# Kernel tuning notes

Measured on AMD Instinct MI355X. Metric: run time of the kernel, lower is better.

The kernel has to match this reference:

```python
import jax, jax.numpy as jnp
import numpy as np

D_IN = 768
D_OUT = 768
NUM_HEADS = 12
HEAD_DIM = D_OUT // NUM_HEADS


def setup_inputs() -> dict:
    key = jax.random.key(0)
    ks = jax.random.split(key, 6)
    s = 1.0 / np.sqrt(D_IN)
    X = jax.random.normal(ks[0], (4, 2048, D_IN), dtype=jnp.float32)
    Wq = jax.random.uniform(ks[1], (D_IN, D_OUT), jnp.float32, -s, s)
    Wk = jax.random.uniform(ks[2], (D_IN, D_OUT), jnp.float32, -s, s)
    Wv = jax.random.uniform(ks[3], (D_IN, D_OUT), jnp.float32, -s, s)
    Wo = jax.random.uniform(ks[4], (D_OUT, D_OUT), jnp.float32, -s, s)
    bo = jax.random.uniform(ks[5], (D_OUT,), jnp.float32, -s, s)
    return {"X": X, "Wq": Wq, "Wk": Wk, "Wv": Wv, "Wo": Wo, "bo": bo}


def reference(X, Wq, Wk, Wv, Wo, bo):
    b, n, _ = X.shape
    # QKV projections, split heads -> [b, h, n, d]
    def split(t):
        return t.reshape(b, n, NUM_HEADS, HEAD_DIM).transpose(0, 2, 1, 3)
    q = split(X @ Wq)
    k = split(X @ Wk)
    v = split(X @ Wv)
    scores = jnp.einsum('bhqd,bhkd->bhqk', q, k) / np.sqrt(HEAD_DIM).astype(np.float32)
    causal = jnp.triu(jnp.ones((n, n), dtype=bool), k=1)
    scores = jnp.where(causal, -jnp.inf, scores)
    attn = jax.nn.softmax(scores, axis=-1)  # dropout p=0 -> identity
    ctx = jnp.einsum('bhqk,bhkd->bhqd', attn, v)
    ctx = ctx.transpose(0, 2, 1, 3).reshape(b, n, D_OUT)
    return ctx @ Wo + bo
```

## Files before the change

kernel.cpp:

```cpp
#include <hip/hip_runtime.h>
#include <stdint.h>

#define B_  4
#define N_  2048
#define D_  768
#define H_  12
#define HD_ 64
#define M_  (B_*N_)

typedef short bf8 __attribute__((ext_vector_type(8)));
typedef float f32x4 __attribute__((ext_vector_type(4)));

static __device__ __forceinline__ unsigned short f2bf(float f) {
    unsigned u = __float_as_uint(f);
    unsigned r = u + 0x7fffu + ((u >> 16) & 1u);
    return (unsigned short)(r >> 16);
}

static __device__ __forceinline__ unsigned pk2bf(float f0, float f1) {
    return ((__float_as_uint(f1) + 0x8000u) & 0xFFFF0000u) |
           ((__float_as_uint(f0) + 0x8000u) >> 16);
}

#if __has_builtin(__builtin_amdgcn_exp2f)
#define EXP2(x) __builtin_amdgcn_exp2f(x)
#else
#define EXP2(x) exp2f(x)
#endif

#define GLOAD_LDS16(gptr, lptr)                                                   \
    __builtin_amdgcn_global_load_lds(                                             \
        (const __attribute__((address_space(1))) void*)(gptr),                    \
        (__attribute__((address_space(3))) void*)(lptr), 16, 0, 0)

#define QSCALE 0.1803368801111204f

__global__ __launch_bounds__(256) void convert_x(const float* __restrict__ X,
                                                 unsigned short* __restrict__ Xb) {
    const size_t i = ((size_t)blockIdx.x * 256 + threadIdx.x) * 8;
    const float4 a = *(const float4*)(X + i);
    const float4 b = *(const float4*)(X + i + 4);
    ushort4 lo, hi;
    lo.x = f2bf(a.x); lo.y = f2bf(a.y); lo.z = f2bf(a.z); lo.w = f2bf(a.w);
    hi.x = f2bf(b.x); hi.y = f2bf(b.y); hi.z = f2bf(b.z); hi.w = f2bf(b.w);
    *(ushort4*)(Xb + i)     = lo;
    *(ushort4*)(Xb + i + 4) = hi;
}

__global__ __launch_bounds__(256) void transpose_w(
    const float* __restrict__ Wq, const float* __restrict__ Wk,
    const float* __restrict__ Wv, const float* __restrict__ Wo,
    unsigned short* __restrict__ Wqt, unsigned short* __restrict__ Wkt,
    unsigned short* __restrict__ Wvt, unsigned short* __restrict__ Wot)
{
    __shared__ float tile[32][33];
    const int z = blockIdx.z;
    const float* W = (z == 0) ? Wq : (z == 1) ? Wk : (z == 2) ? Wv : Wo;
    unsigned short* Wt = (z == 0) ? Wqt : (z == 1) ? Wkt : (z == 2) ? Wvt : Wot;
    const int k0 = blockIdx.x * 32, n0 = blockIdx.y * 32;
    const int tx = threadIdx.x & 31, ty = threadIdx.x >> 5;
    #pragma unroll
    for (int i = 0; i < 4; ++i)
        tile[ty + 8 * i][tx] = W[(size_t)(k0 + ty + 8 * i) * D_ + n0 + tx];
    __syncthreads();
    #pragma unroll
    for (int i = 0; i < 4; ++i)
        Wt[(size_t)(n0 + ty + 8 * i) * D_ + k0 + tx] = f2bf(tile[tx][ty + 8 * i]);
}

__global__ __launch_bounds__(256) void qkv_mfma(
    const unsigned short* __restrict__ Xb,
    const unsigned short* __restrict__ Wqt, const unsigned short* __restrict__ Wkt,
    const unsigned short* __restrict__ Wvt,
    unsigned short* __restrict__ Qb, unsigned short* __restrict__ Kb,
    unsigned short* __restrict__ Vt)
{
    __shared__ unsigned short As[128 * 32];
    __shared__ unsigned short Bs[128 * 32];

    const int t = threadIdx.x;
    const int wave = t >> 6, lane = t & 63;
    const int col = lane & 15, quad = lane >> 4;
    const int wm = (wave & 1) * 64, wn = (wave >> 1) * 64;

    const int m0 = blockIdx.x * 128;
    const int n0 = blockIdx.y * 128;
    const int mat = blockIdx.z;
    const unsigned short* Wt = (mat == 0) ? Wqt : (mat == 1) ? Wkt : Wvt;

    const unsigned short* Ag0 = Xb + (size_t)(m0 + (t >> 2)) * D_ + (t & 3) * 8;
    const unsigned short* Ag1 = Ag0 + (size_t)64 * D_;
    const unsigned short* Bg0 = Wt + (size_t)(n0 + (t >> 2)) * D_ + (t & 3) * 8;
    const unsigned short* Bg1 = Bg0 + (size_t)64 * D_;
    unsigned short* AsW0 = As + wave * 512;
    unsigned short* AsW1 = As + 2048 + wave * 512;
    unsigned short* BsW0 = Bs + wave * 512;
    unsigned short* BsW1 = Bs + 2048 + wave * 512;

    f32x4 acc[4][4] = {};

    for (int k0 = 0; k0 < D_; k0 += 32) {
        __syncthreads();
        GLOAD_LDS16(Ag0 + k0, AsW0);
        GLOAD_LDS16(Ag1 + k0, AsW1);
        GLOAD_LDS16(Bg0 + k0, BsW0);
        GLOAD_LDS16(Bg1 + k0, BsW1);
        __syncthreads();

        bf8 a[4], b[4];
        #pragma unroll
        for (int i = 0; i < 4; ++i)
            a[i] = *(const bf8*)(As + (wm + i * 16 + col) * 32 + quad * 8);
        #pragma unroll
        for (int j = 0; j < 4; ++j)
            b[j] = *(const bf8*)(Bs + (wn + j * 16 + col) * 32 + quad * 8);
        #pragma unroll
        for (int i = 0; i < 4; ++i)
            #pragma unroll
            for (int j = 0; j < 4; ++j)
                acc[i][j] = __builtin_amdgcn_mfma_f32_16x16x32_bf16(a[i], b[j], acc[i][j], 0, 0, 0);
    }

    if (mat != 2) {
        unsigned short* Out = (mat == 0) ? Qb : Kb;
        const float qsc = (mat == 0) ? QSCALE : 1.0f;
        #pragma unroll
        for (int j = 0; j < 4; ++j) {
            const int n = n0 + wn + j * 16 + col;
            const int h = n >> 6, d = n & 63;
            #pragma unroll
            for (int i = 0; i < 4; ++i) {
                const int mb = m0 + wm + i * 16 + quad * 4;
                const int bb = mb >> 11, nn = mb & (N_ - 1);
                unsigned short* op = Out + ((size_t)(bb * H_ + h) * N_ + nn) * HD_ + d;
                #pragma unroll
                for (int r = 0; r < 4; ++r) op[(size_t)r * HD_] = f2bf(acc[i][j][r] * qsc);
            }
        }
    } else {
        #pragma unroll
        for (int j = 0; j < 4; ++j) {
            const int n = n0 + wn + j * 16 + col;
            const int h = n >> 6, d = n & 63;
            #pragma unroll
            for (int i = 0; i < 4; ++i) {
                const int mb = m0 + wm + i * 16 + quad * 4;
                const int bb = mb >> 11, nn = mb & (N_ - 1);
                ushort4 pk;
                pk.x = f2bf(acc[i][j][0]); pk.y = f2bf(acc[i][j][1]);
                pk.z = f2bf(acc[i][j][2]); pk.w = f2bf(acc[i][j][3]);
                *(ushort4*)(Vt + ((size_t)(bb * H_ + h) * HD_ + d) * N_ + nn) = pk;
            }
        }
    }
}

#define PS 72

static __device__ __forceinline__ void qk_softmax(
    const bf8 (&ka)[4][2], bf8 qb0, bf8 qb1,
    int k0, int q, bool mask, float& lpart,
    unsigned short* Pw, int col, int quad)
{
    f32x4 s[4] = {};
    #pragma unroll
    for (int kc = 0; kc < 4; ++kc) {
        s[kc] = __builtin_amdgcn_mfma_f32_16x16x32_bf16(ka[kc][0], qb0, s[kc], 0, 0, 0);
        s[kc] = __builtin_amdgcn_mfma_f32_16x16x32_bf16(ka[kc][1], qb1, s[kc], 0, 0, 0);
    }

    float p[4][4];
    if (mask) {
        #pragma unroll
        for (int kc = 0; kc < 4; ++kc)
            #pragma unroll
            for (int r = 0; r < 4; ++r) {
                const int key = k0 + kc * 16 + quad * 4 + r;
                p[kc][r] = EXP2((key > q) ? -INFINITY : s[kc][r]);
            }
    } else {
        #pragma unroll
        for (int kc = 0; kc < 4; ++kc)
            #pragma unroll
            for (int r = 0; r < 4; ++r) p[kc][r] = EXP2(s[kc][r]);
    }

    #pragma unroll
    for (int kc = 0; kc < 4; ++kc)
        #pragma unroll
        for (int r = 0; r < 4; ++r) lpart += p[kc][r];

    #pragma unroll
    for (int kc = 0; kc < 4; ++kc) {
        uint2 pk;
        pk.x = pk2bf(p[kc][0], p[kc][1]);
        pk.y = pk2bf(p[kc][2], p[kc][3]);
        *(uint2*)(Pw + col * PS + kc * 16 + quad * 4) = pk;
    }
}

static __device__ __forceinline__ void pv_acc(
    const unsigned short* Pw, const bf8 (&va)[4][2],
    f32x4 (&o)[4], int col, int quad)
{
    const bf8 pb0 = *(const bf8*)(Pw + col * PS + quad * 8);
    const bf8 pb1 = *(const bf8*)(Pw + col * PS + 32 + quad * 8);
    #pragma unroll
    for (int dc = 0; dc < 4; ++dc) {
        o[dc] = __builtin_amdgcn_mfma_f32_16x16x32_bf16(va[dc][0], pb0, o[dc], 0, 0, 0);
        o[dc] = __builtin_amdgcn_mfma_f32_16x16x32_bf16(va[dc][1], pb1, o[dc], 0, 0, 0);
    }
}

__global__ __launch_bounds__(256, 3) void attn_mfma(
    const unsigned short* __restrict__ Qb,
    const unsigned short* __restrict__ Kb,
    const unsigned short* __restrict__ Vt,
    unsigned short* __restrict__ Ctxb)
{
    __shared__ unsigned short Kl[64 * PS];
    __shared__ unsigned short Vl[64 * PS];
    __shared__ unsigned short Pl[4][16 * PS];

    const int t = threadIdx.x;
    const int wave = t >> 6;
    const int lane = t & 63;
    const int col  = lane & 15;
    const int quad = lane >> 4;

    const int bid = blockIdx.x;
    const int bh  = bid >> 4;
    const int x   = bid & 15;
    const int tl  = x, th = 31 - x;
    const int q0L = tl * 64 + wave * 16;
    const int q0H = th * 64 + wave * 16;
    const int qL  = q0L + col;
    const int qH  = q0H + col;

    const unsigned short* Kp = Kb + (size_t)bh * N_ * HD_;
    const unsigned short* Vp = Vt + (size_t)bh * HD_ * N_;
    const unsigned short* QpL = Qb + ((size_t)bh * N_ + q0L) * HD_;
    const unsigned short* QpH = Qb + ((size_t)bh * N_ + q0H) * HD_;

    const bf8 qbL0 = *(const bf8*)(QpL + (size_t)col * HD_ + quad * 8);
    const bf8 qbL1 = *(const bf8*)(QpL + (size_t)col * HD_ + 32 + quad * 8);
    const bf8 qbH0 = *(const bf8*)(QpH + (size_t)col * HD_ + quad * 8);
    const bf8 qbH1 = *(const bf8*)(QpH + (size_t)col * HD_ + 32 + quad * 8);

    f32x4 oL[4] = {}, oH[4] = {};
    float lL = 0.f, lH = 0.f;

    unsigned short* Pw = &Pl[wave][0];

    const int srow = t >> 3;
    const int scol = (t & 7) * 8;
    const unsigned short* Kg = Kp + (size_t)srow * HD_ + scol;
    const unsigned short* Vg = Vp + (size_t)srow * N_ + scol;
    unsigned short* KlD0 = Kl + srow * PS + scol;
    unsigned short* KlD1 = Kl + (srow + 32) * PS + scol;
    unsigned short* VlD0 = Vl + srow * PS + scol;
    unsigned short* VlD1 = Vl + (srow + 32) * PS + scol;

    uint4 kr0 = *(const uint4*)(Kg);
    uint4 kr1 = *(const uint4*)(Kg + (size_t)32 * HD_);
    uint4 vr0 = *(const uint4*)(Vg);
    uint4 vr1 = *(const uint4*)(Vg + (size_t)32 * N_);

    const int iters = 32 - x;
    for (int kt = 0; kt < iters; ++kt) {
        const int k0 = kt * 64;
        const bool actL = (kt <= tl);

        *(uint4*)KlD0 = kr0;
        *(uint4*)KlD1 = kr1;
        *(uint4*)VlD0 = vr0;
        *(uint4*)VlD1 = vr1;
        __syncthreads();

        if (kt + 1 < iters) {
            const size_t k1 = (size_t)(k0 + 64);
            kr0 = *(const uint4*)(Kg + k1 * HD_);
            kr1 = *(const uint4*)(Kg + (k1 + 32) * HD_);
            vr0 = *(const uint4*)(Vg + k1);
            vr1 = *(const uint4*)(Vg + (size_t)32 * N_ + k1);
        }

        bf8 ka[4][2];
        #pragma unroll
        for (int kc = 0; kc < 4; ++kc) {
            ka[kc][0] = *(const bf8*)(Kl + (kc * 16 + col) * PS + quad * 8);
            ka[kc][1] = *(const bf8*)(Kl + (kc * 16 + col) * PS + 32 + quad * 8);
        }

        qk_softmax(ka, qbH0, qbH1, k0, qH, kt == th, lH, Pw, col, quad);

        bf8 va[4][2];
        #pragma unroll
        for (int dc = 0; dc < 4; ++dc) {
            va[dc][0] = *(const bf8*)(Vl + (dc * 16 + col) * PS + quad * 8);
            va[dc][1] = *(const bf8*)(Vl + (dc * 16 + col) * PS + 32 + quad * 8);
        }

        pv_acc(Pw, va, oH, col, quad);

        if (actL) {
            qk_softmax(ka, qbL0, qbL1, k0, qL, kt == tl, lL, Pw, col, quad);
            pv_acc(Pw, va, oL, col, quad);
        }

        __syncthreads();
    }

    const int b = bh / H_;
    const int h = bh % H_;
    {
        float l = lH;
        l += __shfl_xor(l, 16, 64);
        l += __shfl_xor(l, 32, 64);
        const float inv = 1.0f / l;
        unsigned short* cp = Ctxb + ((size_t)(b * N_ + qH)) * D_ + h * HD_;
        #pragma unroll
        for (int dc = 0; dc < 4; ++dc) {
            uint2 pk;
            pk.x = pk2bf(oH[dc][0] * inv, oH[dc][1] * inv);
            pk.y = pk2bf(oH[dc][2] * inv, oH[dc][3] * inv);
            *(uint2*)(cp + dc * 16 + quad * 4) = pk;
        }
    }
    {
        float l = lL;
        l += __shfl_xor(l, 16, 64);
        l += __shfl_xor(l, 32, 64);
        const float inv = 1.0f / l;
        unsigned short* cp = Ctxb + ((size_t)(b * N_ + qL)) * D_ + h * HD_;
        #pragma unroll
        for (int dc = 0; dc < 4; ++dc) {
            uint2 pk;
            pk.x = pk2bf(oL[dc][0] * inv, oL[dc][1] * inv);
            pk.y = pk2bf(oL[dc][2] * inv, oL[dc][3] * inv);
            *(uint2*)(cp + dc * 16 + quad * 4) = pk;
        }
    }
}

__global__ __launch_bounds__(256) void out_mfma(
    const unsigned short* __restrict__ Ctxb,
    const unsigned short* __restrict__ Wot,
    const float* __restrict__ bo,
    float* __restrict__ Out)
{
    __shared__ unsigned short As[128 * 32];
    __shared__ unsigned short Bs[128 * 32];

    const int t = threadIdx.x;
    const int wave = t >> 6, lane = t & 63;
    const int col = lane & 15, quad = lane >> 4;
    const int wm = (wave & 1) * 64, wn = (wave >> 1) * 64;

    const int m0 = blockIdx.x * 128;
    const int n0 = blockIdx.y * 128;

    const unsigned short* Ag0 = Ctxb + (size_t)(m0 + (t >> 2)) * D_ + (t & 3) * 8;
    const unsigned short* Ag1 = Ag0 + (size_t)64 * D_;
    const unsigned short* Bg0 = Wot + (size_t)(n0 + (t >> 2)) * D_ + (t & 3) * 8;
    const unsigned short* Bg1 = Bg0 + (size_t)64 * D_;
    unsigned short* AsW0 = As + wave * 512;
    unsigned short* AsW1 = As + 2048 + wave * 512;
    unsigned short* BsW0 = Bs + wave * 512;
    unsigned short* BsW1 = Bs + 2048 + wave * 512;

    f32x4 acc[4][4] = {};

    for (int k0 = 0; k0 < D_; k0 += 32) {
        __syncthreads();
        GLOAD_LDS16(Ag0 + k0, AsW0);
        GLOAD_LDS16(Ag1 + k0, AsW1);
        GLOAD_LDS16(Bg0 + k0, BsW0);
        GLOAD_LDS16(Bg1 + k0, BsW1);
        __syncthreads();

        bf8 a[4], b[4];
        #pragma unroll
        for (int i = 0; i < 4; ++i)
            a[i] = *(const bf8*)(As + (wm + i * 16 + col) * 32 + quad * 8);
        #pragma unroll
        for (int j = 0; j < 4; ++j)
            b[j] = *(const bf8*)(Bs + (wn + j * 16 + col) * 32 + quad * 8);
        #pragma unroll
        for (int i = 0; i < 4; ++i)
            #pragma unroll
            for (int j = 0; j < 4; ++j)
                acc[i][j] = __builtin_amdgcn_mfma_f32_16x16x32_bf16(a[i], b[j], acc[i][j], 0, 0, 0);
    }

    #pragma unroll
    for (int j = 0; j < 4; ++j) {
        const int n = n0 + wn + j * 16 + col;
        const float bias = bo[n];
        #pragma unroll
        for (int i = 0; i < 4; ++i) {
            const int mb = m0 + wm + i * 16 + quad * 4;
            #pragma unroll
            for (int r = 0; r < 4; ++r)
                Out[(size_t)(mb + r) * D_ + n] = acc[i][j][r] + bias;
        }
    }
}

extern "C" void kernel_launch(void* const* d_in, const int* in_sizes, int n_in,
                              void* d_out, int out_size, void* d_ws, size_t ws_size,
                              hipStream_t stream) {
    const float* X  = (const float*)d_in[0];
    const float* Wq = (const float*)d_in[1];
    const float* Wk = (const float*)d_in[2];
    const float* Wv = (const float*)d_in[3];
    const float* Wo = (const float*)d_in[4];
    const float* bo = (const float*)d_in[5];
    float* out = (float*)d_out;

    const size_t elems = (size_t)M_ * D_;
    const size_t welems = (size_t)D_ * D_;
    unsigned short* Xb  = (unsigned short*)d_ws;
    unsigned short* Wqt = Xb + elems;
    unsigned short* Wkt = Wqt + welems;
    unsigned short* Wvt = Wkt + welems;
    unsigned short* Wot = Wvt + welems;
    unsigned short* Qb  = Wot + welems;
    unsigned short* Kb  = Qb + elems;
    unsigned short* Vt  = Kb + elems;
    unsigned short* Ctxb = Xb;

    convert_x<<<dim3(elems / 2048), 256, 0, stream>>>(X, Xb);
    transpose_w<<<dim3(24, 24, 4), 256, 0, stream>>>(Wq, Wk, Wv, Wo, Wqt, Wkt, Wvt, Wot);

    qkv_mfma<<<dim3(M_ / 128, D_ / 128, 3), 256, 0, stream>>>(Xb, Wqt, Wkt, Wvt, Qb, Kb, Vt);

    attn_mfma<<<dim3(B_ * H_ * 16), 256, 0, stream>>>(Qb, Kb, Vt, Ctxb);

    out_mfma<<<dim3(M_ / 128, D_ / 128), 256, 0, stream>>>(Ctxb, Wot, bo, out);
}
```

Measured before the change: 216.7 us.

## Double-buffer attention K/V tiles, widen GEMM K-step, and vectorize epilogue stores

The attention kernel now double-buffers K and V in LDS with a two-stage register prefetch, which removes the trailing barrier per key tile. The QKV and output GEMMs load 64-wide K slices per barrier pair, and for Q/K and the output GEMM they swap the MFMA operands so each lane holds consecutive output columns, allowing 8-byte bf16 and 16-byte float4 stores instead of scalar strided stores. MFMA sections are also wrapped in s_setprio to favor matrix issue. This doubles LDS use in both attention and GEMM kernels, which may reduce occupancy.

```diff
diff --git a/kernel.cpp b/kernel.cpp
--- a/kernel.cpp
+++ b/kernel.cpp
@@ -75,8 +75,8 @@
     unsigned short* __restrict__ Qb, unsigned short* __restrict__ Kb,
     unsigned short* __restrict__ Vt)
 {
-    __shared__ unsigned short As[128 * 32];
-    __shared__ unsigned short Bs[128 * 32];
+    __shared__ unsigned short As[8192];
+    __shared__ unsigned short Bs[8192];
 
     const int t = threadIdx.x;
     const int wave = t >> 6, lane = t & 63;
@@ -87,54 +87,69 @@
     const int n0 = blockIdx.y * 128;
     const int mat = blockIdx.z;
     const unsigned short* Wt = (mat == 0) ? Wqt : (mat == 1) ? Wkt : Wvt;
-
-    const unsigned short* Ag0 = Xb + (size_t)(m0 + (t >> 2)) * D_ + (t & 3) * 8;
-    const unsigned short* Ag1 = Ag0 + (size_t)64 * D_;
-    const unsigned short* Bg0 = Wt + (size_t)(n0 + (t >> 2)) * D_ + (t & 3) * 8;
-    const unsigned short* Bg1 = Bg0 + (size_t)64 * D_;
-    unsigned short* AsW0 = As + wave * 512;
-    unsigned short* AsW1 = As + 2048 + wave * 512;
-    unsigned short* BsW0 = Bs + wave * 512;
-    unsigned short* BsW1 = Bs + 2048 + wave * 512;
+    const bool sw = (mat != 2);
+
+    const unsigned short* Ag = Xb + (size_t)(m0 + (t >> 2)) * D_ + (t & 3) * 8;
+    const unsigned short* Bg = Wt + (size_t)(n0 + (t >> 2)) * D_ + (t & 3) * 8;
+    unsigned short* AsD = As + t * 8;
+    unsigned short* BsD = Bs + t * 8;
 
     f32x4 acc[4][4] = {};
 
-    for (int k0 = 0; k0 < D_; k0 += 32) {
+    for (int k0 = 0; k0 < D_; k0 += 64) {
         __syncthreads();
-        GLOAD_LDS16(Ag0 + k0, AsW0);
-        GLOAD_LDS16(Ag1 + k0, AsW1);
-        GLOAD_LDS16(Bg0 + k0, BsW0);
-        GLOAD_LDS16(Bg1 + k0, BsW1);
+        GLOAD_LDS16(Ag + k0,                        AsD);
+        GLOAD_LDS16(Ag + k0 + 32,                   AsD + 4096);
+        GLOAD_LDS16(Ag + (size_t)64 * D_ + k0,      AsD + 2048);
+        GLOAD_LDS16(Ag + (size_t)64 * D_ + k0 + 32, AsD + 6144);
+        GLOAD_LDS16(Bg + k0,                        BsD);
+        GLOAD_LDS16(Bg + k0 + 32,                   BsD + 4096);
+        GLOAD_LDS16(Bg + (size_t)64 * D_ + k0,      BsD + 2048);
+        GLOAD_LDS16(Bg + (size_t)64 * D_ + k0 + 32, BsD + 6144);
         __syncthreads();
 
-        bf8 a[4], b[4];
-        #pragma unroll
-        for (int i = 0; i < 4; ++i)
-            a[i] = *(const bf8*)(As + (wm + i * 16 + col) * 32 + quad * 8);
-        #pragma unroll
-        for (int j = 0; j < 4; ++j)
-            b[j] = *(const bf8*)(Bs + (wn + j * 16 + col) * 32 + quad * 8);
-        #pragma unroll
-        for (int i = 0; i < 4; ++i)
+        #pragma unroll
+        for (int ks = 0; ks < 2; ++ks) {
+            bf8 a[4], b[4];
+            #pragma unroll
+            for (int i = 0; i < 4; ++i)
+                a[i] = *(const bf8*)(As + ks * 4096 + (wm + i * 16 + col) * 32 + quad * 8);
             #pragma unroll
             for (int j = 0; j < 4; ++j)
-                acc[i][j] = __builtin_amdgcn_mfma_f32_16x16x32_bf16(a[i], b[j], acc[i][j], 0, 0, 0);
-    }
-
-    if (mat != 2) {
+                b[j] = *(const bf8*)(Bs + ks * 4096 + (wn + j * 16 + col) * 32 + quad * 8);
+            if (sw) {
+                #pragma unroll
+                for (int i = 0; i < 4; ++i)
+                    #pragma unroll
+                    for (int j = 0; j < 4; ++j)
+                        acc[i][j] = __builtin_amdgcn_mfma_f32_16x16x32_bf16(b[j], a[i], acc[i][j], 0, 0, 0);
+            } else {
+                #pragma unroll
+                for (int i = 0; i < 4; ++i)
+                    #pragma unroll
+                    for (int j = 0; j < 4; ++j)
+                        acc[i][j] = __builtin_amdgcn_mfma_f32_16x16x32_bf16(a[i], b[j], acc[i][j], 0, 0, 0);
+            }
+        }
+    }
+
+    if (sw) {
         unsigned short* Out = (mat == 0) ? Qb : Kb;
         const float qsc = (mat == 0) ? QSCALE : 1.0f;
         #pragma unroll
-        for (int j = 0; j < 4; ++j) {
-            const int n = n0 + wn + j * 16 + col;
-            const int h = n >> 6, d = n & 63;
-            #pragma unroll
-            for (int i = 0; i < 4; ++i) {
-                const int mb = m0 + wm + i * 16 + quad * 4;
-                const int bb = mb >> 11, nn = mb & (N_ - 1);
-                unsigned short* op = Out + ((size_t)(bb * H_ + h) * N_ + nn) * HD_ + d;
-                #pragma unroll
-                for (int r = 0; r < 4; ++r) op[(size_t)r * HD_] = f2bf(acc[i][j][r] * qsc);
+        for (int i = 0; i < 4; ++i) {
+            const int token = m0 + wm + i * 16 + col;
+            const int bb = token >> 11, nn = token & (N_ - 1);
+            #pragma unroll
+            for (int j = 0; j < 4; ++j) {
+                const int n = n0 + wn + j * 16 + quad * 4;
+                const int h = n >> 6, d = n & 63;
+                ushort4 pk;
+                pk.x = f2bf(acc[i][j][0] * qsc);
+                pk.y = f2bf(acc[i][j][1] * qsc);
+                pk.z = f2bf(acc[i][j][2] * qsc);
+                pk.w = f2bf(acc[i][j][3] * qsc);
+                *(ushort4*)(Out + ((size_t)(bb * H_ + h) * N_ + nn) * HD_ + d) = pk;
             }
         }
     } else {
@@ -163,11 +178,13 @@
     unsigned short* Pw, int col, int quad)
 {
     f32x4 s[4] = {};
+    __builtin_amdgcn_s_setprio(1);
     #pragma unroll
     for (int kc = 0; kc < 4; ++kc) {
         s[kc] = __builtin_amdgcn_mfma_f32_16x16x32_bf16(ka[kc][0], qb0, s[kc], 0, 0, 0);
         s[kc] = __builtin_amdgcn_mfma_f32_16x16x32_bf16(ka[kc][1], qb1, s[kc], 0, 0, 0);
     }
+    __builtin_amdgcn_s_setprio(0);
 
     float p[4][4];
     if (mask) {
@@ -205,11 +222,13 @@
 {
     const bf8 pb0 = *(const bf8*)(Pw + col * PS + quad * 8);
     const bf8 pb1 = *(const bf8*)(Pw + col * PS + 32 + quad * 8);
+    __builtin_amdgcn_s_setprio(1);
     #pragma unroll
     for (int dc = 0; dc < 4; ++dc) {
         o[dc] = __builtin_amdgcn_mfma_f32_16x16x32_bf16(va[dc][0], pb0, o[dc], 0, 0, 0);
         o[dc] = __builtin_amdgcn_mfma_f32_16x16x32_bf16(va[dc][1], pb1, o[dc], 0, 0, 0);
     }
+    __builtin_amdgcn_s_setprio(0);
 }
 
 __global__ __launch_bounds__(256, 3) void attn_mfma(
@@ -218,8 +237,8 @@
     const unsigned short* __restrict__ Vt,
     unsigned short* __restrict__ Ctxb)
 {
-    __shared__ unsigned short Kl[64 * PS];
-    __shared__ unsigned short Vl[64 * PS];
+    __shared__ unsigned short Kl[2][64 * PS];
+    __shared__ unsigned short Vl[2][64 * PS];
     __shared__ unsigned short Pl[4][16 * PS];
 
     const int t = threadIdx.x;
@@ -256,40 +275,53 @@
     const int scol = (t & 7) * 8;
     const unsigned short* Kg = Kp + (size_t)srow * HD_ + scol;
     const unsigned short* Vg = Vp + (size_t)srow * N_ + scol;
-    unsigned short* KlD0 = Kl + srow * PS + scol;
-    unsigned short* KlD1 = Kl + (srow + 32) * PS + scol;
-    unsigned short* VlD0 = Vl + srow * PS + scol;
-    unsigned short* VlD1 = Vl + (srow + 32) * PS + scol;
+    const int kO0 = srow * PS + scol;
+    const int kO1 = (srow + 32) * PS + scol;
+
+    const int iters = 32 - x;
 
     uint4 kr0 = *(const uint4*)(Kg);
     uint4 kr1 = *(const uint4*)(Kg + (size_t)32 * HD_);
     uint4 vr0 = *(const uint4*)(Vg);
     uint4 vr1 = *(const uint4*)(Vg + (size_t)32 * N_);
-
-    const int iters = 32 - x;
+    *(uint4*)(Kl[0] + kO0) = kr0;
+    *(uint4*)(Kl[0] + kO1) = kr1;
+    *(uint4*)(Vl[0] + kO0) = vr0;
+    *(uint4*)(Vl[0] + kO1) = vr1;
+    kr0 = *(const uint4*)(Kg + (size_t)64 * HD_);
+    kr1 = *(const uint4*)(Kg + (size_t)96 * HD_);
+    vr0 = *(const uint4*)(Vg + 64);
+    vr1 = *(const uint4*)(Vg + (size_t)32 * N_ + 64);
+
     for (int kt = 0; kt < iters; ++kt) {
         const int k0 = kt * 64;
         const bool actL = (kt <= tl);
-
-        *(uint4*)KlD0 = kr0;
-        *(uint4*)KlD1 = kr1;
-        *(uint4*)VlD0 = vr0;
-        *(uint4*)VlD1 = vr1;
+        const unsigned short* Kc = Kl[kt & 1];
+        const unsigned short* Vc = Vl[kt & 1];
+        unsigned short* Kn = Kl[(kt + 1) & 1];
+        unsigned short* Vn = Vl[(kt + 1) & 1];
+
         __syncthreads();
 
         if (kt + 1 < iters) {
-            const size_t k1 = (size_t)(k0 + 64);
-            kr0 = *(const uint4*)(Kg + k1 * HD_);
-            kr1 = *(const uint4*)(Kg + (k1 + 32) * HD_);
-            vr0 = *(const uint4*)(Vg + k1);
-            vr1 = *(const uint4*)(Vg + (size_t)32 * N_ + k1);
+            *(uint4*)(Kn + kO0) = kr0;
+            *(uint4*)(Kn + kO1) = kr1;
+            *(uint4*)(Vn + kO0) = vr0;
+            *(uint4*)(Vn + kO1) = vr1;
+        }
+        if (kt + 2 < iters) {
+            const size_t k2 = (size_t)(kt + 2) * 64;
+            kr0 = *(const uint4*)(Kg + k2 * HD_);
+            kr1 = *(const uint4*)(Kg + (k2 + 32) * HD_);
+            vr0 = *(const uint4*)(Vg + k2);
+            vr1 = *(const uint4*)(Vg + (size_t)32 * N_ + k2);
         }
 
         bf8 ka[4][2];
         #pragma unroll
         for (int kc = 0; kc < 4; ++kc) {
-            ka[kc][0] = *(const bf8*)(Kl + (kc * 16 + col) * PS + quad * 8);
-            ka[kc][1] = *(const bf8*)(Kl + (kc * 16 + col) * PS + 32 + quad * 8);
+            ka[kc][0] = *(const bf8*)(Kc + (kc * 16 + col) * PS + quad * 8);
+            ka[kc][1] = *(const bf8*)(Kc + (kc * 16 + col) * PS + 32 + quad * 8);
         }
 
         qk_softmax(ka, qbH0, qbH1, k0, qH, kt == th, lH, Pw, col, quad);
@@ -297,8 +329,8 @@
         bf8 va[4][2];
         #pragma unroll
         for (int dc = 0; dc < 4; ++dc) {
-            va[dc][0] = *(const bf8*)(Vl + (dc * 16 + col) * PS + quad * 8);
-            va[dc][1] = *(const bf8*)(Vl + (dc * 16 + col) * PS + 32 + quad * 8);
+            va[dc][0] = *(const bf8*)(Vc + (dc * 16 + col) * PS + quad * 8);
+            va[dc][1] = *(const bf8*)(Vc + (dc * 16 + col) * PS + 32 + quad * 8);
         }
 
         pv_acc(Pw, va, oH, col, quad);
@@ -307,8 +339,6 @@
             qk_softmax(ka, qbL0, qbL1, k0, qL, kt == tl, lL, Pw, col, quad);
             pv_acc(Pw, va, oL, col, quad);
         }
-
-        __syncthreads();
     }
 
     const int b = bh / H_;
@@ -349,8 +379,8 @@
     const float* __restrict__ bo,
     float* __restrict__ Out)
 {
-    __shared__ unsigned short As[128 * 32];
-    __shared__ unsigned short Bs[128 * 32];
+    __shared__ unsigned short As[8192];
+    __shared__ unsigned short Bs[8192];
 
     const int t = threadIdx.x;
     const int wave = t >> 6, lane = t & 63;
@@ -360,49 +390,55 @@
     const int m0 = blockIdx.x * 128;
     const int n0 = blockIdx.y * 128;
 
-    const unsigned short* Ag0 = Ctxb + (size_t)(m0 + (t >> 2)) * D_ + (t & 3) * 8;
-    const unsigned short* Ag1 = Ag0 + (size_t)64 * D_;
-    const unsigned short* Bg0 = Wot + (size_t)(n0 + (t >> 2)) * D_ + (t & 3) * 8;
-    const unsigned short* Bg1 = Bg0 + (size_t)64 * D_;
-    unsigned short* AsW0 = As + wave * 512;
-    unsigned short* AsW1 = As + 2048 + wave * 512;
-    unsigned short* BsW0 = Bs + wave * 512;
-    unsigned short* BsW1 = Bs + 2048 + wave * 512;
+    const unsigned short* Ag = Ctxb + (size_t)(m0 + (t >> 2)) * D_ + (t & 3) * 8;
+    const unsigned short* Bg = Wot + (size_t)(n0 + (t >> 2)) * D_ + (t & 3) * 8;
+    unsigned short* AsD = As + t * 8;
+    unsigned short* BsD = Bs + t * 8;
 
     f32x4 acc[4][4] = {};
 
-    for (int k0 = 0; k0 < D_; k0 += 32) {
+    for (int k0 = 0; k0 < D_; k0 += 64) {
         __syncthreads();
-        GLOAD_LDS16(Ag0 + k0, AsW0);
-        GLOAD_LDS16(Ag1 + k0, AsW1);
-        GLOAD_LDS16(Bg0 + k0, BsW0);
-        GLOAD_LDS16(Bg1 + k0, BsW1);
+        GLOAD_LDS16(Ag + k0,                        AsD);
+        GLOAD_LDS16(Ag + k0 + 32,                   AsD + 4096);
+        GLOAD_LDS16(Ag + (size_t)64 * D_ + k0,      AsD + 2048);
+        GLOAD_LDS16(Ag + (size_t)64 * D_ + k0 + 32, AsD + 6144);
+        GLOAD_LDS16(Bg + k0,                        BsD);
+        GLOAD_LDS16(Bg + k0 + 32,                   BsD + 4096);
+        GLOAD_LDS16(Bg + (size_t)64 * D_ + k0,      BsD + 2048);
+        GLOAD_LDS16(Bg + (size_t)64 * D_ + k0 + 32, BsD + 6144);
         __syncthreads();
 
-        bf8 a[4], b[4];
-        #pragma unroll
-        for (int i = 0; i < 4; ++i)
-            a[i] = *(const bf8*)(As + (wm + i * 16 + col) * 32 + quad * 8);
-        #pragma unroll
-        for (int j = 0; j < 4; ++j)
-            b[j] = *(const bf8*)(Bs + (wn + j * 16 + col) * 32 + quad * 8);
-        #pragma unroll
-        for (int i = 0; i < 4; ++i)
+        #pragma unroll
+        for (int ks = 0; ks < 2; ++ks) {
+            bf8 a[4], b[4];
+            #pragma unroll
+            for (int i = 0; i < 4; ++i)
+                a[i] = *(const bf8*)(As + ks * 4096 + (wm + i * 16 + col) * 32 + quad * 8);
             #pragma unroll
             for (int j = 0; j < 4; ++j)
-                acc[i][j] = __builtin_amdgcn_mfma_f32_16x16x32_bf16(a[i], b[j], acc[i][j], 0, 0, 0);
-    }
-
-    #pragma unroll
-    for (int j = 0; j < 4; ++j) {
-        const int n = n0 + wn + j * 16 + col;
-        const float bias = bo[n];
-        #pragma unroll
-        for (int i = 0; i < 4; ++i) {
-            const int mb = m0 + wm + i * 16 + quad * 4;
-            #pragma unroll
-            for (int r = 0; r < 4; ++r)
-                Out[(size_t)(mb + r) * D_ + n] = acc[i][j][r] + bias;
+                b[j] = *(const bf8*)(Bs + ks * 4096 + (wn + j * 16 + col) * 32 + quad * 8);
+            #pragma unroll
+            for (int i = 0; i < 4; ++i)
+                #pragma unroll
+                for (int j = 0; j < 4; ++j)
+                    acc[i][j] = __builtin_amdgcn_mfma_f32_16x16x32_bf16(b[j], a[i], acc[i][j], 0, 0, 0);
+        }
+    }
+
+    #pragma unroll
+    for (int i = 0; i < 4; ++i) {
+        const int m = m0 + wm + i * 16 + col;
+        #pragma unroll
+        for (int j = 0; j < 4; ++j) {
+            const int n = n0 + wn + j * 16 + quad * 4;
+            const float4 bias = *(const float4*)(bo + n);
+            float4 o;
+            o.x = acc[i][j][0] + bias.x;
+            o.y = acc[i][j][1] + bias.y;
+            o.z = acc[i][j][2] + bias.z;
+            o.w = acc[i][j][3] + bias.w;
+            *(float4*)(Out + (size_t)m * D_ + n) = o;
         }
     }
 }
```

Measured after the change: 212.5 us. Within noise of the previous version (-2.0%).
